# Performance work log

Measured on AMD Instinct MI355X. Metric: run time of the kernel, lower is better.

## Reference

```python
import jax, jax.numpy as jnp
import numpy as np

N_NODES = 50000
N_EDGES = 800000
IN_DIM, HID_DIM, OUT_DIM = 768, 512, 256


def setup_inputs() -> dict:
    key = jax.random.key(0)
    k1, k2, k3, k4, k5 = jax.random.split(key, 5)
    x = jax.random.normal(k1, (N_NODES, IN_DIM), dtype=jnp.float32)
    edge_index = jax.random.randint(k2, (2, N_EDGES), 0, N_NODES, dtype=jnp.int64)
    # GCNConv params (glorot-ish init)
    W1 = jax.random.normal(k3, (IN_DIM, HID_DIM), dtype=jnp.float32) / np.sqrt(IN_DIM)
    b1 = jnp.zeros((HID_DIM,), dtype=jnp.float32)
    W2 = jax.random.normal(k4, (HID_DIM, OUT_DIM), dtype=jnp.float32) / np.sqrt(HID_DIM)
    b2 = jnp.zeros((OUT_DIM,), dtype=jnp.float32)
    return {"x": x, "edge_index": edge_index, "W1": W1, "b1": b1, "W2": W2, "b2": b2}


def gcn_conv(x, W, b, src, dst, n_nodes):
    """PyG GCNConv: add self-loops, symmetric degree norm, linear, scatter-add, bias."""
    h = x @ W  # [N, F_out]
    loop = jnp.arange(n_nodes, dtype=src.dtype)
    s = jnp.concatenate([src, loop])  # sources incl. self-loops
    d = jnp.concatenate([dst, loop])  # destinations incl. self-loops
    deg = jax.ops.segment_sum(jnp.ones_like(d, dtype=h.dtype), d, num_segments=n_nodes)
    dinv = jnp.where(deg > 0, jax.lax.rsqrt(deg), 0.0)
    norm = dinv[s] * dinv[d]  # [E+N]
    msgs = h[s] * norm[:, None]  # gather + scale (largest intermediate)
    out = jax.ops.segment_sum(msgs, d, num_segments=n_nodes)  # scatter-add
    return out + b


def reference(x, edge_index, W1, b1, W2, b2):
    src, dst = edge_index[0], edge_index[1]
    n = x.shape[0]
    h = gcn_conv(x, W1, b1, src, dst, n)
    h = jax.nn.relu(h)  # dropout is identity in eval mode
    out = gcn_conv(h, W2, b2, src, dst, n)
    return out
```

## Files before the change

kernel.cpp:

```cpp
#include <hip/hip_runtime.h>

#define N_NODES 50000
#define N_EDGES 800000
#define IN_DIM  768
#define HID_DIM 512
#define OUT_DIM 256
#define M_PAD   50048

typedef __attribute__((ext_vector_type(8))) short shortx8;
typedef __attribute__((ext_vector_type(4))) short shortx4;
typedef __attribute__((ext_vector_type(4))) float floatx4;

#define AS1 __attribute__((address_space(1)))
#define AS3 __attribute__((address_space(3)))

__device__ __forceinline__ unsigned short f2bf_rne(float f) {
    unsigned int u = __float_as_uint(f);
    unsigned int r = u + 0x7FFFu + ((u >> 16) & 1u);
    return (unsigned short)(r >> 16);
}
__device__ __forceinline__ float bf2f(unsigned short h) {
    return __uint_as_float(((unsigned int)h) << 16);
}

__global__ void count_deg_kernel(const int* __restrict__ dst, int* __restrict__ deg,
                                 int n_edges) {
    int e = blockIdx.x * blockDim.x + threadIdx.x;
    if (e < n_edges) atomicAdd(&deg[dst[e]], 1);
}

#define SCAN_B 256
#define N_SCAN_BLOCKS ((N_NODES + SCAN_B - 1) / SCAN_B)

__global__ void block_sum_kernel(const int* __restrict__ deg, int* __restrict__ partials,
                                 int n) {
    __shared__ int sm[SCAN_B];
    int i = blockIdx.x * SCAN_B + threadIdx.x;
    sm[threadIdx.x] = (i < n) ? deg[i] : 0;
    __syncthreads();
    for (int off = SCAN_B / 2; off > 0; off >>= 1) {
        if (threadIdx.x < off) sm[threadIdx.x] += sm[threadIdx.x + off];
        __syncthreads();
    }
    if (threadIdx.x == 0) partials[blockIdx.x] = sm[0];
}

__global__ void scan_partials_kernel(const int* __restrict__ partials,
                                     int* __restrict__ bases, int nb) {
    __shared__ int sm[SCAN_B];
    int v = (threadIdx.x < nb) ? partials[threadIdx.x] : 0;
    sm[threadIdx.x] = v;
    __syncthreads();
    for (int off = 1; off < SCAN_B; off <<= 1) {
        int t = (threadIdx.x >= off) ? sm[threadIdx.x - off] : 0;
        __syncthreads();
        sm[threadIdx.x] += t;
        __syncthreads();
    }
    if (threadIdx.x < nb) bases[threadIdx.x] = sm[threadIdx.x] - v;
}

__global__ void finalize_scan_kernel(const int* __restrict__ deg, const int* __restrict__ bases,
                                     int* __restrict__ offsets, int* __restrict__ cursor,
                                     float* __restrict__ dinv, int n) {
    __shared__ int sm[SCAN_B];
    int i = blockIdx.x * SCAN_B + threadIdx.x;
    int v = (i < n) ? deg[i] : 0;
    sm[threadIdx.x] = v;
    __syncthreads();
    for (int off = 1; off < SCAN_B; off <<= 1) {
        int t = (threadIdx.x >= off) ? sm[threadIdx.x - off] : 0;
        __syncthreads();
        sm[threadIdx.x] += t;
        __syncthreads();
    }
    if (i < n) {
        int incl = bases[blockIdx.x] + sm[threadIdx.x];
        int o = incl - v;
        offsets[i] = o;
        cursor[i]  = o;
        dinv[i]    = rsqrtf((float)(v + 1));
        if (i == n - 1) offsets[n] = incl;
    }
}

__global__ void fill_csr_kernel(const int* __restrict__ src, const int* __restrict__ dst,
                                int* __restrict__ cursor, int* __restrict__ csr_src,
                                int n_edges) {
    int e = blockIdx.x * blockDim.x + threadIdx.x;
    if (e < n_edges) {
        int p = atomicAdd(&cursor[dst[e]], 1);
        csr_src[p] = src[e];
    }
}

__global__ void convert_split_kernel(const float* __restrict__ x,
                                     unsigned short* __restrict__ xhi,
                                     unsigned short* __restrict__ xlo,
                                     long long n4) {
    long long i = (long long)blockIdx.x * blockDim.x + threadIdx.x;
    if (i >= n4) return;
    float4 v = *reinterpret_cast<const float4*>(x + i * 4);
    ushort4 h, l;
    h.x = f2bf_rne(v.x); l.x = f2bf_rne(v.x - bf2f(h.x));
    h.y = f2bf_rne(v.y); l.y = f2bf_rne(v.y - bf2f(h.y));
    h.z = f2bf_rne(v.z); l.z = f2bf_rne(v.z - bf2f(h.z));
    h.w = f2bf_rne(v.w); l.w = f2bf_rne(v.w - bf2f(h.w));
    *reinterpret_cast<ushort4*>(xhi + i * 4) = h;
    *reinterpret_cast<ushort4*>(xlo + i * 4) = l;
}

__global__ void transpose_split_kernel(const float* __restrict__ W,
                                       unsigned short* __restrict__ Whi,
                                       unsigned short* __restrict__ Wlo,
                                       int K, int N) {
    __shared__ float tile[32][33];
    int n0 = blockIdx.x * 32, k0 = blockIdx.y * 32;
    int tx = threadIdx.x, ty = threadIdx.y;
    tile[ty][tx] = W[(size_t)(k0 + ty) * N + n0 + tx];
    __syncthreads();
    float v = tile[tx][ty];
    unsigned short h = f2bf_rne(v);
    size_t o = (size_t)(n0 + ty) * K + k0 + tx;
    Whi[o] = h;
    Wlo[o] = f2bf_rne(v - bf2f(h));
}

#define GBK 32

__global__ __launch_bounds__(256)
void gemm_bf16x3_kernel(const unsigned short* __restrict__ Ahi,
                        const unsigned short* __restrict__ Alo,
                        const unsigned short* __restrict__ Bhi,
                        const unsigned short* __restrict__ Blo,
                        const float* __restrict__ dinv,
                        unsigned short* __restrict__ C,
                        int M, int N, int K) {
    __shared__ __align__(16) unsigned short As[2][128][GBK];
    __shared__ __align__(16) unsigned short Bs[2][128][GBK];

    const int tid  = threadIdx.x;
    const int lane = tid & 63;
    const int wave = tid >> 6;
    const int rowBase = blockIdx.y * 128;
    const int colBase = blockIdx.x * 128;

    const unsigned short* gsrc =
        (wave == 0) ? Ahi : (wave == 1) ? Alo : (wave == 2) ? Bhi : Blo;
    unsigned short* lbase =
        (wave == 0) ? &As[0][0][0] : (wave == 1) ? &As[1][0][0]
      : (wave == 2) ? &Bs[0][0][0] : &Bs[1][0][0];
    const int rbase = (wave < 2) ? rowBase : colBase;
    const size_t laneRowOff = (size_t)(rbase + (lane >> 2)) * K + (lane & 3) * 8;

    const int m0 = (wave & 1) * 64;
    const int n0 = (wave >> 1) * 64;
    const int r16 = lane & 15;
    const int kq  = (lane >> 4) * 8;

    floatx4 acc[4][4] = {};

    for (int k0 = 0; k0 < K; k0 += GBK) {
#pragma unroll
        for (int j = 0; j < 8; j++) {
            const unsigned short* g = gsrc + laneRowOff + (size_t)(j * 16) * K + k0;
            __builtin_amdgcn_global_load_lds((const AS1 void*)g,
                                             (AS3 void*)(lbase + j * 16 * GBK),
                                             16, 0, 0);
        }
        __syncthreads();

        shortx8 ah[4], al[4], bh[4], bl[4];
#pragma unroll
        for (int i = 0; i < 4; i++) {
            ah[i] = *reinterpret_cast<const shortx8*>(&As[0][m0 + i * 16 + r16][kq]);
            al[i] = *reinterpret_cast<const shortx8*>(&As[1][m0 + i * 16 + r16][kq]);
            bh[i] = *reinterpret_cast<const shortx8*>(&Bs[0][n0 + i * 16 + r16][kq]);
            bl[i] = *reinterpret_cast<const shortx8*>(&Bs[1][n0 + i * 16 + r16][kq]);
        }
#pragma unroll
        for (int i = 0; i < 4; i++)
#pragma unroll
            for (int j = 0; j < 4; j++) {
                acc[i][j] = __builtin_amdgcn_mfma_f32_16x16x32_bf16(ah[i], bh[j], acc[i][j], 0, 0, 0);
                acc[i][j] = __builtin_amdgcn_mfma_f32_16x16x32_bf16(ah[i], bl[j], acc[i][j], 0, 0, 0);
                acc[i][j] = __builtin_amdgcn_mfma_f32_16x16x32_bf16(al[i], bh[j], acc[i][j], 0, 0, 0);
            }
        __syncthreads();
    }

#pragma unroll
    for (int i = 0; i < 4; i++) {
        int rsub = rowBase + m0 + i * 16 + (lane >> 4) * 4;
#pragma unroll
        for (int j = 0; j < 4; j++) {
            int col = colBase + n0 + j * 16 + r16;
#pragma unroll
            for (int r = 0; r < 4; r++) {
                int row = rsub + r;
                if (row < M) C[(size_t)row * N + col] = f2bf_rne(acc[i][j][r] * dinv[row]);
            }
        }
    }
}

__global__ __launch_bounds__(64)
void aggregate1_kernel(const unsigned short* __restrict__ hs, const int* __restrict__ offsets,
                       const int* __restrict__ csr_src, const float* __restrict__ dinv,
                       const float* __restrict__ bias,
                       unsigned short* __restrict__ yhi,
                       unsigned short* __restrict__ ylo) {
    __shared__ int idxs[64];
    const int node = blockIdx.x;
    const int c = threadIdx.x * 8;
    const unsigned short* hp = hs + c;

    float acc[8];
    {
        shortx8 r = *reinterpret_cast<const shortx8*>(hp + (size_t)node * HID_DIM);
#pragma unroll
        for (int q = 0; q < 8; q++) acc[q] = bf2f((unsigned short)r[q]);
    }
    int beg = offsets[node], end = offsets[node + 1];
    for (int base = beg; base < end; base += 64) {
        int cnt = min(64, end - base);
        __syncthreads();
        if ((int)threadIdx.x < cnt) idxs[threadIdx.x] = csr_src[base + threadIdx.x];
        __syncthreads();
        int j = 0;
        for (; j + 8 <= cnt; j += 8) {
            shortx8 r0 = *reinterpret_cast<const shortx8*>(hp + (size_t)idxs[j + 0] * HID_DIM);
            shortx8 r1 = *reinterpret_cast<const shortx8*>(hp + (size_t)idxs[j + 1] * HID_DIM);
            shortx8 r2 = *reinterpret_cast<const shortx8*>(hp + (size_t)idxs[j + 2] * HID_DIM);
            shortx8 r3 = *reinterpret_cast<const shortx8*>(hp + (size_t)idxs[j + 3] * HID_DIM);
            shortx8 r4 = *reinterpret_cast<const shortx8*>(hp + (size_t)idxs[j + 4] * HID_DIM);
            shortx8 r5 = *reinterpret_cast<const shortx8*>(hp + (size_t)idxs[j + 5] * HID_DIM);
            shortx8 r6 = *reinterpret_cast<const shortx8*>(hp + (size_t)idxs[j + 6] * HID_DIM);
            shortx8 r7 = *reinterpret_cast<const shortx8*>(hp + (size_t)idxs[j + 7] * HID_DIM);
#pragma unroll
            for (int q = 0; q < 8; q++)
                acc[q] += ((bf2f((unsigned short)r0[q]) + bf2f((unsigned short)r1[q]))
                         + (bf2f((unsigned short)r2[q]) + bf2f((unsigned short)r3[q])))
                        + ((bf2f((unsigned short)r4[q]) + bf2f((unsigned short)r5[q]))
                         + (bf2f((unsigned short)r6[q]) + bf2f((unsigned short)r7[q])));
        }
        for (; j < cnt; j++) {
            shortx8 r = *reinterpret_cast<const shortx8*>(hp + (size_t)idxs[j] * HID_DIM);
#pragma unroll
            for (int q = 0; q < 8; q++) acc[q] += bf2f((unsigned short)r[q]);
        }
    }
    float dv = dinv[node];
    floatx4 b0 = *reinterpret_cast<const floatx4*>(bias + c);
    floatx4 b1 = *reinterpret_cast<const floatx4*>(bias + c + 4);
    shortx8 h8, l8;
#pragma unroll
    for (int q = 0; q < 8; q++) {
        float bq = (q < 4) ? b0[q] : b1[q - 4];
        float o = fmaxf(acc[q] * dv + bq, 0.f);
        unsigned short h = f2bf_rne(o);
        h8[q] = (short)h;
        l8[q] = (short)f2bf_rne(o - bf2f(h));
    }
    __builtin_nontemporal_store(h8, reinterpret_cast<shortx8*>(yhi + (size_t)node * HID_DIM + c));
    __builtin_nontemporal_store(l8, reinterpret_cast<shortx8*>(ylo + (size_t)node * HID_DIM + c));
}

__global__ __launch_bounds__(64)
void aggregate2_kernel(const unsigned short* __restrict__ hs, const int* __restrict__ offsets,
                       const int* __restrict__ csr_src, const float* __restrict__ dinv,
                       const float* __restrict__ bias, float* __restrict__ out) {
    __shared__ int idxs[64];
    const int node = blockIdx.x;
    const int c = threadIdx.x * 4;
    const unsigned short* hp = hs + c;

    float acc[4];
    {
        shortx4 r = *reinterpret_cast<const shortx4*>(hp + (size_t)node * OUT_DIM);
#pragma unroll
        for (int q = 0; q < 4; q++) acc[q] = bf2f((unsigned short)r[q]);
    }
    int beg = offsets[node], end = offsets[node + 1];
    for (int base = beg; base < end; base += 64) {
        int cnt = min(64, end - base);
        __syncthreads();
        if ((int)threadIdx.x < cnt) idxs[threadIdx.x] = csr_src[base + threadIdx.x];
        __syncthreads();
        int j = 0;
        for (; j + 8 <= cnt; j += 8) {
            shortx4 r0 = *reinterpret_cast<const shortx4*>(hp + (size_t)idxs[j + 0] * OUT_DIM);
            shortx4 r1 = *reinterpret_cast<const shortx4*>(hp + (size_t)idxs[j + 1] * OUT_DIM);
            shortx4 r2 = *reinterpret_cast<const shortx4*>(hp + (size_t)idxs[j + 2] * OUT_DIM);
            shortx4 r3 = *reinterpret_cast<const shortx4*>(hp + (size_t)idxs[j + 3] * OUT_DIM);
            shortx4 r4 = *reinterpret_cast<const shortx4*>(hp + (size_t)idxs[j + 4] * OUT_DIM);
            shortx4 r5 = *reinterpret_cast<const shortx4*>(hp + (size_t)idxs[j + 5] * OUT_DIM);
            shortx4 r6 = *reinterpret_cast<const shortx4*>(hp + (size_t)idxs[j + 6] * OUT_DIM);
            shortx4 r7 = *reinterpret_cast<const shortx4*>(hp + (size_t)idxs[j + 7] * OUT_DIM);
#pragma unroll
            for (int q = 0; q < 4; q++)
                acc[q] += ((bf2f((unsigned short)r0[q]) + bf2f((unsigned short)r1[q]))
                         + (bf2f((unsigned short)r2[q]) + bf2f((unsigned short)r3[q])))
                        + ((bf2f((unsigned short)r4[q]) + bf2f((unsigned short)r5[q]))
                         + (bf2f((unsigned short)r6[q]) + bf2f((unsigned short)r7[q])));
        }
        for (; j < cnt; j++) {
            shortx4 r = *reinterpret_cast<const shortx4*>(hp + (size_t)idxs[j] * OUT_DIM);
#pragma unroll
            for (int q = 0; q < 4; q++) acc[q] += bf2f((unsigned short)r[q]);
        }
    }
    float dv = dinv[node];
    floatx4 b = *reinterpret_cast<const floatx4*>(bias + c);
    floatx4 o = { acc[0] * dv + b[0], acc[1] * dv + b[1],
                  acc[2] * dv + b[2], acc[3] * dv + b[3] };
    __builtin_nontemporal_store(o, reinterpret_cast<floatx4*>(out + (size_t)node * OUT_DIM + c));
}

extern "C" void kernel_launch(void* const* d_in, const int* in_sizes, int n_in,
                              void* d_out, int out_size, void* d_ws, size_t ws_size,
                              hipStream_t stream) {
    const float* x    = (const float*)d_in[0];
    const int*   edge = (const int*)d_in[1];
    const float* W1   = (const float*)d_in[2];
    const float* b1   = (const float*)d_in[3];
    const float* W2   = (const float*)d_in[4];
    const float* b2   = (const float*)d_in[5];
    float* out = (float*)d_out;

    const int* src = edge;
    const int* dst = edge + N_EDGES;

    char*  ws  = (char*)d_ws;
    size_t off = 0;
    auto alloc = [&](size_t bytes) -> void* {
        void* p = ws + off;
        off += (bytes + 255) & ~(size_t)255;
        return p;
    };
    int*   deg      = (int*)alloc((size_t)N_NODES * 4);
    float* dinv     = (float*)alloc((size_t)N_NODES * 4);
    int*   offsets  = (int*)alloc((size_t)(N_NODES + 1) * 4);
    int*   cursor   = (int*)alloc((size_t)N_NODES * 4);
    int*   csr_src  = (int*)alloc((size_t)N_EDGES * 4);
    int*   partials = (int*)alloc((size_t)N_SCAN_BLOCKS * 4);
    int*   bases    = (int*)alloc((size_t)N_SCAN_BLOCKS * 4);
    unsigned short* xhi   = (unsigned short*)alloc((size_t)M_PAD * IN_DIM * 2);
    unsigned short* xlo   = (unsigned short*)alloc((size_t)M_PAD * IN_DIM * 2);
    unsigned short* w1thi = (unsigned short*)alloc((size_t)HID_DIM * IN_DIM * 2);
    unsigned short* w1tlo = (unsigned short*)alloc((size_t)HID_DIM * IN_DIM * 2);
    unsigned short* w2thi = (unsigned short*)alloc((size_t)OUT_DIM * HID_DIM * 2);
    unsigned short* w2tlo = (unsigned short*)alloc((size_t)OUT_DIM * HID_DIM * 2);
    unsigned short* hs = (unsigned short*)alloc((size_t)N_NODES * HID_DIM * 2);

    unsigned short* y1hi = xhi;
    unsigned short* y1lo = xlo;

    hipMemsetAsync(deg, 0, (size_t)N_NODES * 4, stream);
    count_deg_kernel<<<(N_EDGES + 255) / 256, 256, 0, stream>>>(dst, deg, N_EDGES);
    block_sum_kernel<<<N_SCAN_BLOCKS, SCAN_B, 0, stream>>>(deg, partials, N_NODES);
    scan_partials_kernel<<<1, SCAN_B, 0, stream>>>(partials, bases, N_SCAN_BLOCKS);
    finalize_scan_kernel<<<N_SCAN_BLOCKS, SCAN_B, 0, stream>>>(deg, bases, offsets, cursor,
                                                               dinv, N_NODES);
    fill_csr_kernel<<<(N_EDGES + 255) / 256, 256, 0, stream>>>(src, dst, cursor, csr_src, N_EDGES);

    long long n4x = (long long)N_NODES * IN_DIM / 4;
    convert_split_kernel<<<(int)((n4x + 255) / 256), 256, 0, stream>>>(x, xhi, xlo, n4x);
    transpose_split_kernel<<<dim3(HID_DIM / 32, IN_DIM / 32), dim3(32, 32), 0, stream>>>(
        W1, w1thi, w1tlo, IN_DIM, HID_DIM);
    transpose_split_kernel<<<dim3(OUT_DIM / 32, HID_DIM / 32), dim3(32, 32), 0, stream>>>(
        W2, w2thi, w2tlo, HID_DIM, OUT_DIM);

    gemm_bf16x3_kernel<<<dim3(HID_DIM / 128, M_PAD / 128), 256, 0, stream>>>(
        xhi, xlo, w1thi, w1tlo, dinv, hs, N_NODES, HID_DIM, IN_DIM);
    aggregate1_kernel<<<N_NODES, 64, 0, stream>>>(
        hs, offsets, csr_src, dinv, b1, y1hi, y1lo);

    gemm_bf16x3_kernel<<<dim3(OUT_DIM / 128, M_PAD / 128), 256, 0, stream>>>(
        y1hi, y1lo, w2thi, w2tlo, dinv, hs, N_NODES, OUT_DIM, HID_DIM);
    aggregate2_kernel<<<N_NODES, 64, 0, stream>>>(
        hs, offsets, csr_src, dinv, b2, out);
}
```

Measured before the change: 781.6 us.

## Double-buffer GEMM LDS tiles, swizzle LDS layout, and remap blocks across XCDs

The bf16x3 GEMM now keeps two LDS stages and prefetches the next K-slice with global_load_lds while the current slice is consumed by MFMAs, dropping one barrier per iteration. It also XOR-swizzles the 16-byte column groups in LDS so fragment reads hit fewer bank conflicts. Block IDs are remapped so consecutive tiles land on the same XCD for better L2 reuse. This doubles LDS use, which may lower occupancy, and relies on the loop's single barrier to keep the buffers ordered.

```diff
diff --git a/kernel.cpp b/kernel.cpp
--- a/kernel.cpp
+++ b/kernel.cpp
@@ -136,57 +136,79 @@
                         const float* __restrict__ dinv,
                         unsigned short* __restrict__ C,
                         int M, int N, int K) {
-    __shared__ __align__(16) unsigned short As[2][128][GBK];
-    __shared__ __align__(16) unsigned short Bs[2][128][GBK];
+    __shared__ __align__(16) unsigned short As[2][2][128][GBK];
+    __shared__ __align__(16) unsigned short Bs[2][2][128][GBK];
 
     const int tid  = threadIdx.x;
     const int lane = tid & 63;
     const int wave = tid >> 6;
-    const int rowBase = blockIdx.y * 128;
-    const int colBase = blockIdx.x * 128;
+
+    const int gx   = gridDim.x;
+    const int nwg  = gx * gridDim.y;
+    const int blin = blockIdx.y * gx + blockIdx.x;
+    const int qq   = nwg >> 3, rr = nwg & 7;
+    const int xcd  = blin & 7, idx = blin >> 3;
+    const int tt   = (xcd < rr ? xcd * (qq + 1) : rr * (qq + 1) + (xcd - rr) * qq) + idx;
+    const int rowBase = (tt / gx) * 128;
+    const int colBase = (tt % gx) * 128;
 
     const unsigned short* gsrc =
         (wave == 0) ? Ahi : (wave == 1) ? Alo : (wave == 2) ? Bhi : Blo;
-    unsigned short* lbase =
-        (wave == 0) ? &As[0][0][0] : (wave == 1) ? &As[1][0][0]
-      : (wave == 2) ? &Bs[0][0][0] : &Bs[1][0][0];
+    unsigned short* l0 =
+        (wave == 0) ? &As[0][0][0][0] : (wave == 1) ? &As[0][1][0][0]
+      : (wave == 2) ? &Bs[0][0][0][0] : &Bs[0][1][0][0];
+    unsigned short* l1 = l0 + 2 * 128 * GBK;
     const int rbase = (wave < 2) ? rowBase : colBase;
-    const size_t laneRowOff = (size_t)(rbase + (lane >> 2)) * K + (lane & 3) * 8;
-
-    const int m0 = (wave & 1) * 64;
-    const int n0 = (wave >> 1) * 64;
+    const int cg = ((lane & 3) ^ ((lane >> 3) & 3)) * 8;
+    const size_t laneRowOff = (size_t)(rbase + (lane >> 2)) * K + cg;
+
+    const int m0  = (wave & 1) * 64;
+    const int n0  = (wave >> 1) * 64;
     const int r16 = lane & 15;
-    const int kq  = (lane >> 4) * 8;
+    const int kswz = ((lane >> 4) ^ ((r16 >> 1) & 3)) * 8;
 
     floatx4 acc[4][4] = {};
 
+#pragma unroll
+    for (int j = 0; j < 8; j++) {
+        const unsigned short* g = gsrc + laneRowOff + (size_t)(j * 16) * K;
+        __builtin_amdgcn_global_load_lds((const AS1 void*)g,
+                                         (AS3 void*)(l0 + j * 16 * GBK), 16, 0, 0);
+    }
+    __syncthreads();
+
+    int cur = 0;
     for (int k0 = 0; k0 < K; k0 += GBK) {
-#pragma unroll
-        for (int j = 0; j < 8; j++) {
-            const unsigned short* g = gsrc + laneRowOff + (size_t)(j * 16) * K + k0;
-            __builtin_amdgcn_global_load_lds((const AS1 void*)g,
-                                             (AS3 void*)(lbase + j * 16 * GBK),
-                                             16, 0, 0);
-        }
-        __syncthreads();
-
-        shortx8 ah[4], al[4], bh[4], bl[4];
+        if (k0 + GBK < K) {
+            unsigned short* dstp = cur ? l0 : l1;
+#pragma unroll
+            for (int j = 0; j < 8; j++) {
+                const unsigned short* g =
+                    gsrc + laneRowOff + (size_t)(j * 16) * K + (k0 + GBK);
+                __builtin_amdgcn_global_load_lds((const AS1 void*)g,
+                                                 (AS3 void*)(dstp + j * 16 * GBK),
+                                                 16, 0, 0);
+            }
+        }
+
+        shortx8 ah[4], al[4], bh[4], bv[4];
 #pragma unroll
         for (int i = 0; i < 4; i++) {
-            ah[i] = *reinterpret_cast<const shortx8*>(&As[0][m0 + i * 16 + r16][kq]);
-            al[i] = *reinterpret_cast<const shortx8*>(&As[1][m0 + i * 16 + r16][kq]);
-            bh[i] = *reinterpret_cast<const shortx8*>(&Bs[0][n0 + i * 16 + r16][kq]);
-            bl[i] = *reinterpret_cast<const shortx8*>(&Bs[1][n0 + i * 16 + r16][kq]);
+            ah[i] = *reinterpret_cast<const shortx8*>(&As[cur][0][m0 + i * 16 + r16][kswz]);
+            al[i] = *reinterpret_cast<const shortx8*>(&As[cur][1][m0 + i * 16 + r16][kswz]);
+            bh[i] = *reinterpret_cast<const shortx8*>(&Bs[cur][0][n0 + i * 16 + r16][kswz]);
+            bv[i] = *reinterpret_cast<const shortx8*>(&Bs[cur][1][n0 + i * 16 + r16][kswz]);
         }
 #pragma unroll
         for (int i = 0; i < 4; i++)
 #pragma unroll
             for (int j = 0; j < 4; j++) {
                 acc[i][j] = __builtin_amdgcn_mfma_f32_16x16x32_bf16(ah[i], bh[j], acc[i][j], 0, 0, 0);
-                acc[i][j] = __builtin_amdgcn_mfma_f32_16x16x32_bf16(ah[i], bl[j], acc[i][j], 0, 0, 0);
+                acc[i][j] = __builtin_amdgcn_mfma_f32_16x16x32_bf16(ah[i], bv[j], acc[i][j], 0, 0, 0);
                 acc[i][j] = __builtin_amdgcn_mfma_f32_16x16x32_bf16(al[i], bh[j], acc[i][j], 0, 0, 0);
             }
         __syncthreads();
+        cur ^= 1;
     }
 
 #pragma unroll
```

After: 796.8 us. Within noise of the previous version (+1.9%).

## Swizzle LDS layout, remap blocks across XCDs, and raise GEMM occupancy

Applied to the files above, without the earlier changes.

The split-bf16 GEMM now stores its LDS tiles with an XOR swizzle on the 16-byte column group, applied the same way on the global-to-LDS load and on the fragment reads, to cut bank conflicts. Block IDs are remapped so each XCD gets a contiguous range of output tiles, which should improve L2 reuse of the A and B panels. Launch bounds now request 4 waves per SIMD, and the A fragments are loaded per row-tile instead of all at once to lower register pressure. The tighter register budget could force spills, and the swizzle has to match exactly between the write and read paths.

```diff
diff --git a/kernel.cpp b/kernel.cpp
--- a/kernel.cpp
+++ b/kernel.cpp
@@ -128,7 +128,7 @@
 
 #define GBK 32
 
-__global__ __launch_bounds__(256)
+__global__ __launch_bounds__(256, 4)
 void gemm_bf16x3_kernel(const unsigned short* __restrict__ Ahi,
                         const unsigned short* __restrict__ Alo,
                         const unsigned short* __restrict__ Bhi,
@@ -142,8 +142,15 @@
     const int tid  = threadIdx.x;
     const int lane = tid & 63;
     const int wave = tid >> 6;
-    const int rowBase = blockIdx.y * 128;
-    const int colBase = blockIdx.x * 128;
+
+    const int gx   = gridDim.x;
+    const int nwg  = gx * gridDim.y;
+    const int blin = blockIdx.y * gx + blockIdx.x;
+    const int qq   = nwg >> 3, rr = nwg & 7;
+    const int xcd  = blin & 7, idx = blin >> 3;
+    const int tt   = (xcd < rr ? xcd * (qq + 1) : rr * (qq + 1) + (xcd - rr) * qq) + idx;
+    const int rowBase = (tt / gx) * 128;
+    const int colBase = (tt % gx) * 128;
 
     const unsigned short* gsrc =
         (wave == 0) ? Ahi : (wave == 1) ? Alo : (wave == 2) ? Bhi : Blo;
@@ -151,12 +158,13 @@
         (wave == 0) ? &As[0][0][0] : (wave == 1) ? &As[1][0][0]
       : (wave == 2) ? &Bs[0][0][0] : &Bs[1][0][0];
     const int rbase = (wave < 2) ? rowBase : colBase;
-    const size_t laneRowOff = (size_t)(rbase + (lane >> 2)) * K + (lane & 3) * 8;
-
-    const int m0 = (wave & 1) * 64;
-    const int n0 = (wave >> 1) * 64;
+    const int cg = ((lane & 3) ^ ((lane >> 3) & 3)) * 8;
+    const size_t laneRowOff = (size_t)(rbase + (lane >> 2)) * K + cg;
+
+    const int m0  = (wave & 1) * 64;
+    const int n0  = (wave >> 1) * 64;
     const int r16 = lane & 15;
-    const int kq  = (lane >> 4) * 8;
+    const int kswz = ((lane >> 4) ^ ((r16 >> 1) & 3)) * 8;
 
     floatx4 acc[4][4] = {};
 
@@ -170,22 +178,23 @@
         }
         __syncthreads();
 
-        shortx8 ah[4], al[4], bh[4], bl[4];
+        shortx8 bh[4], bv[4];
+#pragma unroll
+        for (int j = 0; j < 4; j++) {
+            bh[j] = *reinterpret_cast<const shortx8*>(&Bs[0][n0 + j * 16 + r16][kswz]);
+            bv[j] = *reinterpret_cast<const shortx8*>(&Bs[1][n0 + j * 16 + r16][kswz]);
+        }
 #pragma unroll
         for (int i = 0; i < 4; i++) {
-            ah[i] = *reinterpret_cast<const shortx8*>(&As[0][m0 + i * 16 + r16][kq]);
-            al[i] = *reinterpret_cast<const shortx8*>(&As[1][m0 + i * 16 + r16][kq]);
-            bh[i] = *reinterpret_cast<const shortx8*>(&Bs[0][n0 + i * 16 + r16][kq]);
-            bl[i] = *reinterpret_cast<const shortx8*>(&Bs[1][n0 + i * 16 + r16][kq]);
-        }
-#pragma unroll
-        for (int i = 0; i < 4; i++)
+            shortx8 ah = *reinterpret_cast<const shortx8*>(&As[0][m0 + i * 16 + r16][kswz]);
+            shortx8 al = *reinterpret_cast<const shortx8*>(&As[1][m0 + i * 16 + r16][kswz]);
 #pragma unroll
             for (int j = 0; j < 4; j++) {
-                acc[i][j] = __builtin_amdgcn_mfma_f32_16x16x32_bf16(ah[i], bh[j], acc[i][j], 0, 0, 0);
-                acc[i][j] = __builtin_amdgcn_mfma_f32_16x16x32_bf16(ah[i], bl[j], acc[i][j], 0, 0, 0);
-                acc[i][j] = __builtin_amdgcn_mfma_f32_16x16x32_bf16(al[i], bh[j], acc[i][j], 0, 0, 0);
+                acc[i][j] = __builtin_amdgcn_mfma_f32_16x16x32_bf16(ah, bh[j], acc[i][j], 0, 0, 0);
+                acc[i][j] = __builtin_amdgcn_mfma_f32_16x16x32_bf16(ah, bv[j], acc[i][j], 0, 0, 0);
+                acc[i][j] = __builtin_amdgcn_mfma_f32_16x16x32_bf16(al, bh[j], acc[i][j], 0, 0, 0);
             }
+        }
         __syncthreads();
     }
 
```

New measurement: 760.3 us. 1.03x faster.
